# Optimization experiments

Measured on AMD Instinct MI355X. Metric: run time of the kernel, lower is better.

Reference implementation:

```python
import jax, jax.numpy as jnp
import numpy as np

EMBED = 1024
HEADS = 16
HEAD_DIM = EMBED // HEADS  # 64 quantum wires


def setup_inputs() -> dict:
    key = jax.random.key(0)
    ks = jax.random.split(key, 6)
    s = 1.0 / np.sqrt(EMBED)
    return {
        "x": jax.random.normal(ks[0], (8, 4096, EMBED), dtype=jnp.float32),
        "Wk": jax.random.normal(ks[1], (EMBED, EMBED), dtype=jnp.float32) * s,
        "Wq": jax.random.normal(ks[2], (EMBED, EMBED), dtype=jnp.float32) * s,
        "Wv": jax.random.normal(ks[3], (EMBED, EMBED), dtype=jnp.float32) * s,
        "Wo": jax.random.normal(ks[4], (EMBED, EMBED), dtype=jnp.float32) * s,
        "theta": jax.random.normal(ks[5], (HEAD_DIM,), dtype=jnp.float32),
    }


def reference(x, Wk, Wq, Wv, Wo, theta):
    b, s, _ = x.shape
    # linear projections (torch Linear: y = x @ W^T), split heads -> [b,s,h,d]
    def proj(W):
        return (x @ W.T).reshape(b, s, HEADS, HEAD_DIM)
    k, q, v = proj(Wk), proj(Wq), proj(Wv)
    # QLayer: per-wire RX(x_i) then trainable RX(theta_i) on |0>, measure PauliZ
    # -> <Z_i> = cos(x_i + theta_i) exactly (product state, independent wires).
    k_q = jnp.cos(k + theta)
    q_q = jnp.cos(q + theta)
    v_q = jnp.cos(v + theta)
    # Faithful to source: matmul over last two dims of [b,s,h,d] -> attention
    # across the HEADS axis ([b,s,h,h]), not across sequence.
    scores = jnp.einsum('bsid,bsjd->bsij', q_q, k_q) / jnp.sqrt(
        jnp.asarray(HEAD_DIM, dtype=x.dtype))
    attn = jax.nn.softmax(scores, axis=-1)  # dropout = identity at inference
    out = jnp.einsum('bsij,bsjd->bsid', attn, v_q).reshape(b, s, EMBED)
    return out @ Wo.T
```

## Files before the change

kernel.cpp:

```cpp
#include <hip/hip_runtime.h>
#include <hip/hip_fp16.h>

#define NTOK 32768
#define NE   1024

typedef _Float16 half_t;
typedef _Float16 f16x8 __attribute__((ext_vector_type(8)));
typedef _Float16 f16x4 __attribute__((ext_vector_type(4)));
typedef float    f32x4 __attribute__((ext_vector_type(4)));

typedef __attribute__((address_space(1))) const unsigned int guint;
typedef __attribute__((address_space(3))) unsigned int luint;

__device__ __forceinline__ void async16(const void* g, void* l) {
    __builtin_amdgcn_global_load_lds((guint*)g, (luint*)l, 16, 0, 0);
}

__global__ __launch_bounds__(256) void cvt_f32_f16(const float* __restrict__ s,
                                                   half_t* __restrict__ d, int n) {
    int i = (blockIdx.x * 256 + threadIdx.x) * 8;
    if (i >= n) return;
    float4 a = *(const float4*)(s + i);
    float4 b = *(const float4*)(s + i + 4);
    f16x8 h = {(_Float16)a.x, (_Float16)a.y, (_Float16)a.z, (_Float16)a.w,
               (_Float16)b.x, (_Float16)b.y, (_Float16)b.z, (_Float16)b.w};
    *(f16x8*)(d + i) = h;
}

__global__ __launch_bounds__(256) void cvt4_f32_f16(const float* __restrict__ s0,
                                                    const float* __restrict__ s1,
                                                    const float* __restrict__ s2,
                                                    const float* __restrict__ s3,
                                                    half_t* __restrict__ d) {
    const float* srcs[4] = {s0, s1, s2, s3};
    const float* s = srcs[blockIdx.y];
    int i = (blockIdx.x * 256 + threadIdx.x) * 8;
    float4 a = *(const float4*)(s + i);
    float4 b = *(const float4*)(s + i + 4);
    f16x8 h = {(_Float16)a.x, (_Float16)a.y, (_Float16)a.z, (_Float16)a.w,
               (_Float16)b.x, (_Float16)b.y, (_Float16)b.z, (_Float16)b.w};
    *(f16x8*)(d + (size_t)blockIdx.y * (NE * NE) + i) = h;
}


#define WAITV(N) asm volatile("s_waitcnt vmcnt(" #N ")" ::: "memory")
#define BARRIER()                              \
    do {                                       \
        asm volatile("" ::: "memory");         \
        __builtin_amdgcn_s_barrier();          \
        asm volatile("" ::: "memory");         \
    } while (0)

#define ASC(b, c) (Asm + ((b) * 2 + (c)) * 8192)
#define BSC(b, c) (Bsm + ((b) * 2 + (c)) * 8192)

#define STAGE_A(dst, q, k0)                                                   \
    do {                                                                      \
        _Pragma("unroll") for (int l = 0; l < 2; ++l)                         \
            async16(Ag + (size_t)(l * 128 + (q) * 64 + rr) * K + (k0) + cc,   \
                    (char*)(dst) + l * 8192 + w * 1024);                      \
    } while (0)

#define STAGE_B(dst, r, k0)                                                   \
    do {                                                                      \
        _Pragma("unroll") for (int l = 0; l < 2; ++l)                         \
            async16(Bg + (size_t)((l * 2 + wb) * 64 + (r) * 32 + (rr & 31)) * K + \
                        (k0) + cc,                                            \
                    (char*)(dst) + l * 8192 + w * 1024);                      \
    } while (0)

#define READ_A(dstf, b, q)                                                    \
    do {                                                                      \
        _Pragma("unroll") for (int i = 0; i < 4; ++i)                         \
        _Pragma("unroll") for (int x = 0; x < 2; ++x)                         \
            dstf[i][x] = *(const f16x8*)&ASC(b, q)[(wr * 64 + i * 16 + l16) * 64 + \
                                                   (((x * 4 + quad) ^ sw) * 8)]; \
    } while (0)

#define READ_B(dstf, b, r)                                                    \
    do {                                                                      \
        _Pragma("unroll") for (int i2 = 0; i2 < 2; ++i2)                      \
        _Pragma("unroll") for (int x = 0; x < 2; ++x)                         \
            dstf[i2][x] = *(const f16x8*)&BSC(b, r)[(wc * 32 + i2 * 16 + l16) * 64 + \
                                                    (((x * 4 + quad) ^ sw) * 8)]; \
    } while (0)

#define MMA(af, bf, QA, RB)                                                   \
    do {                                                                      \
        __builtin_amdgcn_s_setprio(1);                                        \
        _Pragma("unroll") for (int i = 0; i < 4; ++i)                         \
        _Pragma("unroll") for (int jj = 0; jj < 2; ++jj)                      \
        _Pragma("unroll") for (int x = 0; x < 2; ++x)                         \
            acc[(QA) * 4 + i][(RB) * 2 + jj] =                                \
                __builtin_amdgcn_mfma_f32_16x16x32_f16(                       \
                    af[i][x], bf[jj][x], acc[(QA) * 4 + i][(RB) * 2 + jj], 0, 0, 0); \
        __builtin_amdgcn_s_setprio(0);                                        \
    } while (0)

template <bool QKV>
__global__ __launch_bounds__(512, 2) void gemm_bt(const half_t* __restrict__ A,
                                                  const half_t* __restrict__ Bbase,
                                                  void* __restrict__ Cout,
                                                  const float* __restrict__ theta) {
    constexpr int K  = 1024;
    constexpr int NT = 16;
    constexpr int J  = QKV ? 12 : 4;
    __shared__ alignas(16) half_t smem[65536];
    half_t* Asm = smem;
    half_t* Bsm = smem + 32768;

    const int id    = blockIdx.x;
    const int xcd   = id & 7;
    const int slot  = id >> 3;
    const int ygrp  = slot / J;
    const int j     = slot - ygrp * J;
    const int mtile = ygrp * 8 + xcd;
    const int zsl   = QKV ? (j >> 2) : 0;
    const int xt    = QKV ? (j & 3) : j;

    const int tid  = threadIdx.x;
    const int w    = tid >> 6;
    const int lane = tid & 63;
    const int quad = lane >> 4;
    const int l16  = lane & 15;
    const int sw   = l16 & 7;
    const int wr   = w >> 2, wc = w & 3;
    const size_t m0 = (size_t)mtile * 256;
    const int    n0 = xt * 256;

    const half_t* Ag = A + m0 * K;
    const half_t* Bg = Bbase + (size_t)zsl * (size_t)(NE * NE) + (size_t)n0 * K;

    const int rr = tid >> 3;
    const int cc = ((tid & 7) ^ (rr & 7)) * 8;
    const int wb = tid >> 8;

    f32x4 acc[8][4];
#pragma unroll
    for (int i = 0; i < 8; ++i)
#pragma unroll
        for (int jj = 0; jj < 4; ++jj) acc[i][jj] = (f32x4){0.f, 0.f, 0.f, 0.f};

    STAGE_A(ASC(0, 0), 0, 0);
    STAGE_B(BSC(0, 0), 0, 0);
    STAGE_B(BSC(0, 1), 1, 0);
    STAGE_A(ASC(0, 1), 1, 0);
    STAGE_A(ASC(1, 0), 0, 64);
    WAITV(6);
    BARRIER();

    f16x8 aF0[4][2], aF1[4][2], bF0[2][2], bF1[2][2];
    READ_A(aF0, 0, 0);
    READ_B(bF0, 0, 0);

    for (int t = 0; t < NT - 1; ++t) {
        const int cur = t & 1, nxt = cur ^ 1;
        const int kn = (t + 1) * 64;
        WAITV(4);
        BARRIER();
        STAGE_B(BSC(nxt, 0), 0, kn);
        MMA(aF0, bF0, 0, 0);
        READ_B(bF1, cur, 1);
        BARRIER();
        WAITV(4);
        BARRIER();
        STAGE_B(BSC(nxt, 1), 1, kn);
        MMA(aF0, bF1, 0, 1);
        READ_A(aF1, cur, 1);
        BARRIER();
        WAITV(4);
        BARRIER();
        STAGE_A(ASC(nxt, 1), 1, kn);
        MMA(aF1, bF1, 1, 1);
        BARRIER();
        WAITV(4);
        BARRIER();
        if (t + 2 < NT) STAGE_A(ASC(cur, 0), 0, kn + 64);
        MMA(aF1, bF0, 1, 0);
        READ_A(aF0, nxt, 0);
        READ_B(bF0, nxt, 0);
        BARRIER();
    }
    {
        WAITV(2);
        BARRIER();
        MMA(aF0, bF0, 0, 0);
        READ_B(bF1, 1, 1);
        BARRIER();
        WAITV(0);
        BARRIER();
        MMA(aF0, bF1, 0, 1);
        READ_A(aF1, 1, 1);
        BARRIER();
        MMA(aF1, bF1, 1, 1);
        MMA(aF1, bF0, 1, 0);
    }
    __syncthreads();

    if (QKV) {
        half_t* Cl = smem;
#pragma unroll
        for (int nt = 0; nt < 4; ++nt) {
            const int col = wc * 64 + nt * 16 + l16;
            const float th = theta[col & 63];
#pragma unroll
            for (int mt = 0; mt < 8; ++mt) {
                const int rowb = wr * 128 + mt * 16 + quad * 4;
#pragma unroll
                for (int r = 0; r < 4; ++r) {
                    const int row = rowb + r;
                    Cl[row * 256 + (col ^ (((row >> 2) & 3) << 4))] =
                        (half_t)__cosf(acc[mt][nt][r] + th);
                }
            }
        }
        __syncthreads();
        half_t* Cg = (half_t*)Cout + (size_t)zsl * ((size_t)NTOK * NE);
#pragma unroll
        for (int it = 0; it < 16; ++it) {
            const int row = it * 16 + (tid >> 5);
            const int seg = tid & 31;
            f16x8 vv = *(const f16x8*)&Cl[row * 256 +
                                          ((seg * 8) ^ (((row >> 2) & 3) << 4))];
            *(f16x8*)&Cg[(m0 + row) * NE + n0 + seg * 8] = vv;
        }
    } else {
        float* ClF = (float*)smem;
        float* Cg  = (float*)Cout;
#pragma unroll
        for (int s = 0; s < 2; ++s) {
            if (wr == s) {
#pragma unroll
                for (int nt = 0; nt < 4; ++nt) {
                    const int col = wc * 64 + nt * 16 + l16;
#pragma unroll
                    for (int mt = 0; mt < 8; ++mt) {
                        const int rowb = mt * 16 + quad * 4;
#pragma unroll
                        for (int r = 0; r < 4; ++r) {
                            const int row = rowb + r;
                            ClF[row * 256 + (col ^ (((row >> 2) & 1) << 4))] =
                                acc[mt][nt][r];
                        }
                    }
                }
            }
            __syncthreads();
#pragma unroll
            for (int it = 0; it < 16; ++it) {
                const int row = it * 8 + (tid >> 6);
                const int seg = tid & 63;
                f32x4 vv = *(const f32x4*)&ClF[row * 256 +
                                               ((seg * 4) ^ (((row >> 2) & 1) << 4))];
                *(f32x4*)&Cg[(m0 + s * 128 + row) * NE + n0 + seg * 4] = vv;
            }
            __syncthreads();
        }
    }
}

__global__ __launch_bounds__(512) void attn_kernel(const half_t* __restrict__ q,
                                                   const half_t* __restrict__ k,
                                                   const half_t* __restrict__ v,
                                                   half_t* __restrict__ out) {
    __shared__ half_t vT[8][64][20];
    __shared__ half_t Pl[8][16][20];
    const int tid  = threadIdx.x;
    const int w    = tid >> 6;
    const int lane = tid & 63;
    const int quad = lane >> 4;
    const int l16  = lane & 15;
    const size_t base = ((size_t)blockIdx.x * 8 + w) * 1024;

    {
        const int h = lane >> 2, d0 = (lane & 3) * 16;
        f16x8 va = *(const f16x8*)(v + base + h * 64 + d0);
        f16x8 vb = *(const f16x8*)(v + base + h * 64 + d0 + 8);
#pragma unroll
        for (int z = 0; z < 8; ++z) {
            vT[w][d0 + z][h]     = va[z];
            vT[w][d0 + 8 + z][h] = vb[z];
        }
    }

    f16x8 aq0 = *(const f16x8*)(q + base + l16 * 64 + quad * 8);
    f16x8 aq1 = *(const f16x8*)(q + base + l16 * 64 + 32 + quad * 8);
    f16x8 bk0 = *(const f16x8*)(k + base + l16 * 64 + quad * 8);
    f16x8 bk1 = *(const f16x8*)(k + base + l16 * 64 + 32 + quad * 8);
    f32x4 S = __builtin_amdgcn_mfma_f32_16x16x32_f16(aq0, bk0, (f32x4){0.f,0.f,0.f,0.f}, 0, 0, 0);
    S = __builtin_amdgcn_mfma_f32_16x16x32_f16(aq1, bk1, S, 0, 0, 0);

#pragma unroll
    for (int r = 0; r < 4; ++r) {
        float s = S[r] * 0.125f;
        float mx = s;
#pragma unroll
        for (int o = 8; o; o >>= 1) mx = fmaxf(mx, __shfl_xor(mx, o));
        float e = __expf(s - mx);
        float sum = e;
#pragma unroll
        for (int o = 8; o; o >>= 1) sum += __shfl_xor(sum, o);
        Pl[w][quad * 4 + r][l16] = (half_t)(e / sum);
    }
    __syncthreads();

    f16x4 ap = *(const f16x4*)&Pl[w][l16][quad * 4];
#pragma unroll
    for (int c = 0; c < 4; ++c) {
        f16x4 bv = *(const f16x4*)&vT[w][c * 16 + l16][quad * 4];
        f32x4 O = __builtin_amdgcn_mfma_f32_16x16x16f16(ap, bv, (f32x4){0.f,0.f,0.f,0.f}, 0, 0, 0);
#pragma unroll
        for (int r = 0; r < 4; ++r)
            out[base + (quad * 4 + r) * 64 + c * 16 + l16] = (half_t)O[r];
    }
}

extern "C" void kernel_launch(void* const* d_in, const int* in_sizes, int n_in,
                              void* d_out, int out_size, void* d_ws, size_t ws_size,
                              hipStream_t stream) {
    const float* x     = (const float*)d_in[0];
    const float* Wk    = (const float*)d_in[1];
    const float* Wq    = (const float*)d_in[2];
    const float* Wv    = (const float*)d_in[3];
    const float* Wo    = (const float*)d_in[4];
    const float* theta = (const float*)d_in[5];

    char* ws = (char*)d_ws;
    half_t* xh  = (half_t*)ws;
    half_t* wh  = (half_t*)(ws + (size_t)(64 << 20));
    half_t* qkv = (half_t*)(ws + (size_t)(72 << 20));

    cvt_f32_f16<<<NTOK * NE / 2048, 256, 0, stream>>>(x, xh, NTOK * NE);
    cvt4_f32_f16<<<dim3(NE * NE / 2048, 4), 256, 0, stream>>>(Wq, Wk, Wv, Wo, wh);

    gemm_bt<true><<<1536, 512, 0, stream>>>(xh, wh, qkv, theta);

    attn_kernel<<<NTOK / 8, 512, 0, stream>>>(qkv, qkv + (size_t)NTOK * NE,
                                              qkv + 2 * (size_t)NTOK * NE, xh);

    gemm_bt<false><<<512, 512, 0, stream>>>(xh, wh + 3 * NE * NE, d_out, nullptr);
}
```

Measured before the change: 554.0 us.

## Store V row-major in LDS, drop block barrier, stage output for vector stores

The attention kernel now writes V to LDS row-major with 16-byte vector stores instead of a scalar transpose. The B operand is gathered with strided scalar LDS reads, and the block-wide __syncthreads is removed because each wave only touches its own LDS slice. The MFMA results are staged back through the same LDS buffer so each lane can write the output with 16-byte global stores instead of scattered 2-byte stores. Intra-wave ordering now relies on explicit lgkmcnt waits, and removing the barrier without a wave-level fence is a correctness risk.

```diff
diff --git a/kernel.cpp b/kernel.cpp
--- a/kernel.cpp
+++ b/kernel.cpp
@@ -263,8 +263,8 @@
                                                    const half_t* __restrict__ k,
                                                    const half_t* __restrict__ v,
                                                    half_t* __restrict__ out) {
-    __shared__ half_t vT[8][64][20];
-    __shared__ half_t Pl[8][16][20];
+    __shared__ alignas(16) half_t vR[8][16][72];
+    __shared__ alignas(16) half_t Pl[8][16][20];
     const int tid  = threadIdx.x;
     const int w    = tid >> 6;
     const int lane = tid & 63;
@@ -276,11 +276,8 @@
         const int h = lane >> 2, d0 = (lane & 3) * 16;
         f16x8 va = *(const f16x8*)(v + base + h * 64 + d0);
         f16x8 vb = *(const f16x8*)(v + base + h * 64 + d0 + 8);
-#pragma unroll
-        for (int z = 0; z < 8; ++z) {
-            vT[w][d0 + z][h]     = va[z];
-            vT[w][d0 + 8 + z][h] = vb[z];
-        }
+        *(f16x8*)&vR[w][h][d0]     = va;
+        *(f16x8*)&vR[w][h][d0 + 8] = vb;
     }
 
     f16x8 aq0 = *(const f16x8*)(q + base + l16 * 64 + quad * 8);
@@ -302,16 +299,37 @@
         for (int o = 8; o; o >>= 1) sum += __shfl_xor(sum, o);
         Pl[w][quad * 4 + r][l16] = (half_t)(e / sum);
     }
-    __syncthreads();
 
     f16x4 ap = *(const f16x4*)&Pl[w][l16][quad * 4];
+    float Of[16];
 #pragma unroll
     for (int c = 0; c < 4; ++c) {
-        f16x4 bv = *(const f16x4*)&vT[w][c * 16 + l16][quad * 4];
+        f16x4 bv;
+#pragma unroll
+        for (int qi = 0; qi < 4; ++qi)
+            bv[qi] = vR[w][quad * 4 + qi][c * 16 + l16];
         f32x4 O = __builtin_amdgcn_mfma_f32_16x16x16f16(ap, bv, (f32x4){0.f,0.f,0.f,0.f}, 0, 0, 0);
 #pragma unroll
+        for (int r = 0; r < 4; ++r) Of[c * 4 + r] = O[r];
+    }
+
+    asm volatile("s_waitcnt lgkmcnt(0)" ::: "memory");
+    __builtin_amdgcn_sched_barrier(0);
+
+#pragma unroll
+    for (int c = 0; c < 4; ++c)
+#pragma unroll
         for (int r = 0; r < 4; ++r)
-            out[base + (quad * 4 + r) * 64 + c * 16 + l16] = (half_t)O[r];
+            vR[w][quad * 4 + r][c * 16 + l16] = (half_t)Of[c * 4 + r];
+
+    asm volatile("s_waitcnt lgkmcnt(0)" ::: "memory");
+    __builtin_amdgcn_sched_barrier(0);
+    {
+        const int rw = lane >> 2, d0 = (lane & 3) * 16;
+        f16x8 oa = *(const f16x8*)&vR[w][rw][d0];
+        f16x8 ob = *(const f16x8*)&vR[w][rw][d0 + 8];
+        *(f16x8*)(out + base + rw * 64 + d0)     = oa;
+        *(f16x8*)(out + base + rw * 64 + d0 + 8) = ob;
     }
 }
 
```

Result: no change. 564.1 us (+1.8%).

## Merge conversion kernels and trim barriers in GEMM main loop

Applied to the files above, without the earlier changes.

Fuses the x and weight fp32-to-fp16 conversion kernels into one launch to save a kernel launch. In the GEMM K-loop it removes several redundant barriers and one wait/barrier pair, and marks the loop unroll 1. Fewer barriers let waves overlap LDS reads, MFMA and async staging more, but this risks LDS read/write races between staging into buffers and fragment reads, which could corrupt results.

```diff
diff --git a/kernel.cpp b/kernel.cpp
--- a/kernel.cpp
+++ b/kernel.cpp
@@ -16,30 +16,32 @@
     __builtin_amdgcn_global_load_lds((guint*)g, (luint*)l, 16, 0, 0);
 }
 
-__global__ __launch_bounds__(256) void cvt_f32_f16(const float* __restrict__ s,
-                                                   half_t* __restrict__ d, int n) {
-    int i = (blockIdx.x * 256 + threadIdx.x) * 8;
-    if (i >= n) return;
+__global__ __launch_bounds__(256) void cvt_all(const float* __restrict__ x,
+                                               const float* __restrict__ w0,
+                                               const float* __restrict__ w1,
+                                               const float* __restrict__ w2,
+                                               const float* __restrict__ w3,
+                                               half_t* __restrict__ dx,
+                                               half_t* __restrict__ dw) {
+    const int id = blockIdx.x;
+    const float* s;
+    half_t* d;
+    int i;
+    if (id < 16384) {
+        s = x; d = dx;
+        i = (id * 256 + threadIdx.x) * 8;
+    } else {
+        const int m = (id - 16384) >> 9;
+        const float* ws[4] = {w0, w1, w2, w3};
+        s = ws[m];
+        d = dw + (size_t)m * (NE * NE);
+        i = (((id - 16384) & 511) * 256 + threadIdx.x) * 8;
+    }
     float4 a = *(const float4*)(s + i);
     float4 b = *(const float4*)(s + i + 4);
     f16x8 h = {(_Float16)a.x, (_Float16)a.y, (_Float16)a.z, (_Float16)a.w,
                (_Float16)b.x, (_Float16)b.y, (_Float16)b.z, (_Float16)b.w};
     *(f16x8*)(d + i) = h;
-}
-
-__global__ __launch_bounds__(256) void cvt4_f32_f16(const float* __restrict__ s0,
-                                                    const float* __restrict__ s1,
-                                                    const float* __restrict__ s2,
-                                                    const float* __restrict__ s3,
-                                                    half_t* __restrict__ d) {
-    const float* srcs[4] = {s0, s1, s2, s3};
-    const float* s = srcs[blockIdx.y];
-    int i = (blockIdx.x * 256 + threadIdx.x) * 8;
-    float4 a = *(const float4*)(s + i);
-    float4 b = *(const float4*)(s + i + 4);
-    f16x8 h = {(_Float16)a.x, (_Float16)a.y, (_Float16)a.z, (_Float16)a.w,
-               (_Float16)b.x, (_Float16)b.y, (_Float16)b.z, (_Float16)b.w};
-    *(f16x8*)(d + (size_t)blockIdx.y * (NE * NE) + i) = h;
 }
 
 
@@ -153,6 +155,7 @@
     READ_A(aF0, 0, 0);
     READ_B(bF0, 0, 0);
 
+#pragma unroll 1
     for (int t = 0; t < NT - 1; ++t) {
         const int cur = t & 1, nxt = cur ^ 1;
         const int kn = (t + 1) * 64;
@@ -161,37 +164,29 @@
         STAGE_B(BSC(nxt, 0), 0, kn);
         MMA(aF0, bF0, 0, 0);
         READ_B(bF1, cur, 1);
-        BARRIER();
         WAITV(4);
         BARRIER();
         STAGE_B(BSC(nxt, 1), 1, kn);
         MMA(aF0, bF1, 0, 1);
         READ_A(aF1, cur, 1);
-        BARRIER();
-        WAITV(4);
-        BARRIER();
         STAGE_A(ASC(nxt, 1), 1, kn);
         MMA(aF1, bF1, 1, 1);
-        BARRIER();
         WAITV(4);
         BARRIER();
         if (t + 2 < NT) STAGE_A(ASC(cur, 0), 0, kn + 64);
         MMA(aF1, bF0, 1, 0);
         READ_A(aF0, nxt, 0);
         READ_B(bF0, nxt, 0);
-        BARRIER();
     }
     {
         WAITV(2);
         BARRIER();
         MMA(aF0, bF0, 0, 0);
         READ_B(bF1, 1, 1);
-        BARRIER();
         WAITV(0);
         BARRIER();
         MMA(aF0, bF1, 0, 1);
         READ_A(aF1, 1, 1);
-        BARRIER();
         MMA(aF1, bF1, 1, 1);
         MMA(aF1, bF0, 1, 0);
     }
@@ -330,8 +325,7 @@
     half_t* wh  = (half_t*)(ws + (size_t)(64 << 20));
     half_t* qkv = (half_t*)(ws + (size_t)(72 << 20));
 
-    cvt_f32_f16<<<NTOK * NE / 2048, 256, 0, stream>>>(x, xh, NTOK * NE);
-    cvt4_f32_f16<<<dim3(NE * NE / 2048, 4), 256, 0, stream>>>(Wq, Wk, Wv, Wo, wh);
+    cvt_all<<<16384 + 4 * 512, 256, 0, stream>>>(x, Wq, Wk, Wv, Wo, xh, wh);
 
     gemm_bt<true><<<1536, 512, 0, stream>>>(xh, wh, qkv, theta);
 
```

Result: no change. 550.3 us (-0.7%).
